# Performance work log

Measured on AMD Instinct MI355X. Metric: run time of the kernel, lower is better.

## Reference

```python
import jax, jax.numpy as jnp
import numpy as np

B, IN_DIM, HV_DIM, NUM_CLASSES = 16384, 2048, 8192, 1000


def setup_inputs() -> dict:
    key = jax.random.key(0)
    kx, kp, kc = jax.random.split(key, 3)
    x = jax.random.normal(kx, (B, IN_DIM), dtype=jnp.float32)
    # +/-1 random projection and class hypervectors (2*bernoulli - 1), as in the torch buffers
    proj = (jax.random.randint(kp, (IN_DIM, HV_DIM), 0, 2) * 2 - 1).astype(jnp.float32)
    class_hv = (jax.random.randint(kc, (HV_DIM, NUM_CLASSES), 0, 2) * 2 - 1).astype(jnp.float32)
    return {"x": x, "proj": proj, "class_hv": class_hv}


def reference(x, proj, class_hv):
    # dense projection -> sign binarize -> binary associative-memory matmul (score_mode='dot')
    hv = x @ proj                                   # [B, HV_DIM]
    hv_bin = jnp.where(hv >= 0, 1.0, -1.0).astype(hv.dtype)
    scores = hv_bin @ class_hv                      # [B, NUM_CLASSES]
    return scores, hv_bin
```

## Files before the change

kernel.cpp:

```cpp
#include <hip/hip_runtime.h>
#include <hip/hip_bf16.h>

typedef _Float16 half8  __attribute__((ext_vector_type(8)));
typedef _Float16 half4_t __attribute__((ext_vector_type(4)));
typedef float    floatx4 __attribute__((ext_vector_type(4)));
typedef int      intx4   __attribute__((ext_vector_type(4)));

#define B_DIM   16384
#define IN_D    2048
#define HV_D    8192
#define NC      1000
#define NCP     1024
#define SCORES_N (B_DIM * NC)

#define GLD16(gp, lp) __builtin_amdgcn_global_load_lds( \
    (const __attribute__((address_space(1))) void*)(gp), \
    (__attribute__((address_space(3))) void*)(lp), 16, 0, 0)

__global__ void k_split(const float* __restrict__ x, _Float16* __restrict__ xh,
                        _Float16* __restrict__ xl) {
    size_t i = (size_t)blockIdx.x * 256 + threadIdx.x;
    floatx4 v = ((const floatx4*)x)[i];
    half4_t h, l;
#pragma unroll
    for (int j = 0; j < 4; ++j) {
        _Float16 hh = (_Float16)v[j];
        h[j] = hh;
        l[j] = (_Float16)(v[j] - (float)hh);
    }
    ((half4_t*)xh)[i] = h;
    ((half4_t*)xl)[i] = l;
}

__global__ void k_transpose_proj(const float* __restrict__ p, _Float16* __restrict__ pT) {
    __shared__ float tile[64][65];
    const int t = threadIdx.x;
    const int nt = blockIdx.x * 64;
    const int kt = blockIdx.y * 64;
    const int tr = t >> 4, tc = (t & 15) * 4;
#pragma unroll
    for (int s = 0; s < 4; ++s) {
        int r = tr + s * 16;
        floatx4 v = *(const floatx4*)&p[(size_t)(kt + r) * HV_D + nt + tc];
        tile[r][tc] = v[0]; tile[r][tc + 1] = v[1];
        tile[r][tc + 2] = v[2]; tile[r][tc + 3] = v[3];
    }
    __syncthreads();
#pragma unroll
    for (int s = 0; s < 4; ++s) {
        int rn = tr + s * 16;
        half4_t o;
#pragma unroll
        for (int j = 0; j < 4; ++j) o[j] = (_Float16)tile[tc + j][rn];
        *(half4_t*)&pT[(size_t)(nt + rn) * IN_D + kt + tc] = o;
    }
}

__global__ void k_pack_class(const float* __restrict__ c, signed char* __restrict__ cT) {
    __shared__ signed char tile[64][68];
    const int t = threadIdx.x;
    const int nt = blockIdx.x * 64;
    const int kt = blockIdx.y * 64;
    const int nl = t & 63;
    const int n = nt + nl;
#pragma unroll
    for (int s = 0; s < 16; ++s) {
        const int kl = s * 4 + (t >> 6);
        signed char v = 0;
        if (n < NC) {
            float f = c[(size_t)(kt + kl) * NC + n];
            v = (f >= 0.f) ? (signed char)1 : (signed char)-1;
        }
        tile[kl][nl] = v;
    }
    __syncthreads();
    const int wn = t >> 2;
    const int wk = (t & 3) * 16;
    intx4 o;
    signed char* ob = (signed char*)&o;
#pragma unroll
    for (int j = 0; j < 16; ++j) ob[j] = tile[wk + j][wn];
    *(intx4*)&cT[(size_t)(nt + wn) * HV_D + kt + wk] = o;
}

__launch_bounds__(256, 2)
__global__ void k_gemm1(const _Float16* __restrict__ xh, const _Float16* __restrict__ xl,
                        const _Float16* __restrict__ pT,
                        float* __restrict__ hv_out, signed char* __restrict__ hvb,
                        int mbase) {
    __shared__ _Float16 sAh[128 * 64];
    __shared__ _Float16 sAl[128 * 64];
    __shared__ _Float16 sB [256 * 64];
    const int t = threadIdx.x;
    const int w = t >> 6, l = t & 63;

    const int orig = blockIdx.y * 32 + blockIdx.x;
    const int lid  = (orig & 7) * 128 + (orig >> 3);
    const int bx = lid & 31, by = lid >> 5;

    const int m0 = mbase + by * 128, n0 = bx * 256;
    const int wm = (w >> 1) * 64, wn = (w & 1) * 128;
    const int lm = l & 15, kq = l >> 4;
    const int srow  = w * 8 + (l >> 3);
    const int scol  = (((l & 7) ^ ((l >> 3) & 7))) * 8;
    const int sbyte = w * 1024 + l * 16;

    floatx4 acc[4][8] = {};

    for (int k0 = 0; k0 < IN_D; k0 += 64) {
        __syncthreads();
#pragma unroll
        for (int i = 0; i < 4; ++i) {
            const size_t ga = (size_t)(m0 + srow + i * 32) * IN_D + k0 + scol;
            const int lo = sbyte + i * 4096;
            GLD16(xh + ga, (char*)sAh + lo);
            GLD16(xl + ga, (char*)sAl + lo);
        }
#pragma unroll
        for (int i = 0; i < 8; ++i) {
            const size_t gb = (size_t)(n0 + srow + i * 32) * IN_D + k0 + scol;
            GLD16(pT + gb, (char*)sB + sbyte + i * 4096);
        }
        __syncthreads();
#pragma unroll
        for (int ks = 0; ks < 2; ++ks) {
            const int csw = ((ks * 4 + kq) ^ (lm & 7)) * 8;
            half8 b[8];
#pragma unroll
            for (int ns = 0; ns < 8; ++ns)
                b[ns] = *(const half8*)&sB[(wn + ns * 16 + lm) * 64 + csw];
#pragma unroll
            for (int ms = 0; ms < 4; ++ms) {
                half8 a = *(const half8*)&sAh[(wm + ms * 16 + lm) * 64 + csw];
#pragma unroll
                for (int ns = 0; ns < 8; ++ns)
                    acc[ms][ns] = __builtin_amdgcn_mfma_f32_16x16x32_f16(a, b[ns], acc[ms][ns], 0, 0, 0);
            }
#pragma unroll
            for (int ms = 0; ms < 4; ++ms) {
                half8 a = *(const half8*)&sAl[(wm + ms * 16 + lm) * 64 + csw];
#pragma unroll
                for (int ns = 0; ns < 8; ++ns)
                    acc[ms][ns] = __builtin_amdgcn_mfma_f32_16x16x32_f16(a, b[ns], acc[ms][ns], 0, 0, 0);
            }
        }
    }

#pragma unroll
    for (int ms = 0; ms < 4; ++ms) {
#pragma unroll
        for (int ns = 0; ns < 8; ++ns) {
            const int m = m0 + wm + ms * 16 + kq * 4;
            const int n = n0 + wn + ns * 16 + lm;
#pragma unroll
            for (int r = 0; r < 4; ++r) {
                const int pos = (acc[ms][ns][r] >= 0.f);
                const size_t o = (size_t)(m + r) * HV_D + n;
                __builtin_nontemporal_store(pos ? 1.f : -1.f, &hv_out[o]);
                hvb[o] = (signed char)(pos ? 1 : -1);
            }
        }
    }
}

__launch_bounds__(256, 4)
__global__ void k_gemm2(const signed char* __restrict__ hvb, const signed char* __restrict__ cT,
                        float* __restrict__ scores) {
    __shared__ signed char sA[64 * 128];
    __shared__ signed char sB[256 * 128];
    const int t = threadIdx.x;
    const int w = t >> 6, l = t & 63;

    const int orig = blockIdx.y * 4 + blockIdx.x;
    const int lid  = (orig & 7) * 128 + (orig >> 3);
    const int bx = lid & 3, by = lid >> 2;

    const int m0 = by * 64, n0 = bx * 256;
    const int wm = (w >> 1) * 32, wn = (w & 1) * 128;
    const int lm = l & 15, kq = l >> 4;
    const int srow  = w * 8 + (l >> 3);
    const int scol  = (((l & 7) ^ ((l >> 3) & 7))) * 16;
    const int sbyte = w * 1024 + l * 16;

    intx4 acc[2][8] = {};

    for (int k0 = 0; k0 < HV_D; k0 += 128) {
        __syncthreads();
#pragma unroll
        for (int i = 0; i < 2; ++i)
            GLD16(hvb + (size_t)(m0 + srow + i * 32) * HV_D + k0 + scol,
                  (char*)sA + sbyte + i * 4096);
#pragma unroll
        for (int i = 0; i < 8; ++i)
            GLD16(cT + (size_t)(n0 + srow + i * 32) * HV_D + k0 + scol,
                  (char*)sB + sbyte + i * 4096);
        __syncthreads();
#pragma unroll
        for (int ks = 0; ks < 2; ++ks) {
            const int csw = ((ks * 4 + kq) ^ (lm & 7)) * 16;
            intx4 b[8];
#pragma unroll
            for (int ns = 0; ns < 8; ++ns)
                b[ns] = *(const intx4*)&sB[(wn + ns * 16 + lm) * 128 + csw];
#pragma unroll
            for (int ms = 0; ms < 2; ++ms) {
                intx4 a = *(const intx4*)&sA[(wm + ms * 16 + lm) * 128 + csw];
#pragma unroll
                for (int ns = 0; ns < 8; ++ns)
                    acc[ms][ns] = __builtin_amdgcn_mfma_i32_16x16x64_i8(a, b[ns], acc[ms][ns], 0, 0, 0);
            }
        }
    }

#pragma unroll
    for (int ms = 0; ms < 2; ++ms) {
#pragma unroll
        for (int ns = 0; ns < 8; ++ns) {
            const int m = m0 + wm + ms * 16 + kq * 4;
            const int n = n0 + wn + ns * 16 + lm;
            if (n < NC) {
#pragma unroll
                for (int r = 0; r < 4; ++r)
                    __builtin_nontemporal_store((float)acc[ms][ns][r],
                                                &scores[(size_t)(m + r) * NC + n]);
            }
        }
    }
}

extern "C" void kernel_launch(void* const* d_in, const int* in_sizes, int n_in,
                              void* d_out, int out_size, void* d_ws, size_t ws_size,
                              hipStream_t stream) {
    const float* x    = (const float*)d_in[0];
    const float* proj = (const float*)d_in[1];
    const float* chv  = (const float*)d_in[2];
    float* out    = (float*)d_out;
    float* scores = out;
    float* hv_out = out + (size_t)SCORES_N;

    char* ws = (char*)d_ws;
    _Float16*    xh  = (_Float16*)(ws);
    _Float16*    xl  = (_Float16*)(ws + (size_t)67108864);
    _Float16*    pT  = (_Float16*)(ws + (size_t)134217728);
    signed char* cT  = (signed char*)(ws + (size_t)167772160);
    signed char* hvb = (signed char*)(ws + (size_t)176160768);

    k_split<<<(B_DIM * IN_D / 4) / 256, 256, 0, stream>>>(x, xh, xl);
    k_transpose_proj<<<dim3(HV_D / 64, IN_D / 64), 256, 0, stream>>>(proj, pT);
    k_pack_class<<<dim3(NCP / 64, HV_D / 64), 256, 0, stream>>>(chv, cT);
    k_gemm1<<<dim3(HV_D / 256, B_DIM / 512), 256, 0, stream>>>(xh, xl, pT, hv_out, hvb, 0);
    k_gemm1<<<dim3(HV_D / 256, B_DIM / 512), 256, 0, stream>>>(xh, xl, pT, hv_out, hvb, 4096);
    k_gemm1<<<dim3(HV_D / 256, B_DIM / 512), 256, 0, stream>>>(xh, xl, pT, hv_out, hvb, 8192);
    k_gemm1<<<dim3(HV_D / 256, B_DIM / 512), 256, 0, stream>>>(xh, xl, pT, hv_out, hvb, 12288);
    k_gemm2<<<dim3(NCP / 256, B_DIM / 64), 256, 0, stream>>>(hvb, cT, scores);
}
```

Measured before the change: 1.697 ms.

## Rewrite projection GEMM as 8-wave double-buffered ping-pong pipeline with single launch

```diff
diff --git a/kernel.cpp b/kernel.cpp
--- a/kernel.cpp
+++ b/kernel.cpp
@@ -83,84 +83,138 @@
     *(intx4*)&cT[(size_t)(nt + wn) * HV_D + kt + wk] = o;
 }
 
-__launch_bounds__(256, 2)
+__launch_bounds__(512, 2)
 __global__ void k_gemm1(const _Float16* __restrict__ xh, const _Float16* __restrict__ xl,
                         const _Float16* __restrict__ pT,
-                        float* __restrict__ hv_out, signed char* __restrict__ hvb,
-                        int mbase) {
-    __shared__ _Float16 sAh[128 * 64];
-    __shared__ _Float16 sAl[128 * 64];
-    __shared__ _Float16 sB [256 * 64];
+                        float* __restrict__ hv_out, signed char* __restrict__ hvb) {
+    __shared__ _Float16 sAh[2][128 * 64];
+    __shared__ _Float16 sAl[2][128 * 64];
+    __shared__ _Float16 sB [2][256 * 64];
     const int t = threadIdx.x;
     const int w = t >> 6, l = t & 63;
-
-    const int orig = blockIdx.y * 32 + blockIdx.x;
-    const int lid  = (orig & 7) * 128 + (orig >> 3);
-    const int bx = lid & 31, by = lid >> 5;
-
-    const int m0 = mbase + by * 128, n0 = bx * 256;
-    const int wm = (w >> 1) * 64, wn = (w & 1) * 128;
+    const int m0 = blockIdx.y * 128, n0 = blockIdx.x * 256;
+    const int wm = (w >> 2) * 64, wn = (w & 3) * 64;
     const int lm = l & 15, kq = l >> 4;
-    const int srow  = w * 8 + (l >> 3);
-    const int scol  = (((l & 7) ^ ((l >> 3) & 7))) * 8;
-    const int sbyte = w * 1024 + l * 16;
-
-    floatx4 acc[4][8] = {};
-
-    for (int k0 = 0; k0 < IN_D; k0 += 64) {
-        __syncthreads();
-#pragma unroll
-        for (int i = 0; i < 4; ++i) {
-            const size_t ga = (size_t)(m0 + srow + i * 32) * IN_D + k0 + scol;
-            const int lo = sbyte + i * 4096;
-            GLD16(xh + ga, (char*)sAh + lo);
-            GLD16(xl + ga, (char*)sAl + lo);
-        }
-#pragma unroll
-        for (int i = 0; i < 8; ++i) {
-            const size_t gb = (size_t)(n0 + srow + i * 32) * IN_D + k0 + scol;
-            GLD16(pT + gb, (char*)sB + sbyte + i * 4096);
-        }
-        __syncthreads();
-#pragma unroll
-        for (int ks = 0; ks < 2; ++ks) {
-            const int csw = ((ks * 4 + kq) ^ (lm & 7)) * 8;
-            half8 b[8];
-#pragma unroll
-            for (int ns = 0; ns < 8; ++ns)
-                b[ns] = *(const half8*)&sB[(wn + ns * 16 + lm) * 64 + csw];
-#pragma unroll
-            for (int ms = 0; ms < 4; ++ms) {
-                half8 a = *(const half8*)&sAh[(wm + ms * 16 + lm) * 64 + csw];
-#pragma unroll
-                for (int ns = 0; ns < 8; ++ns)
-                    acc[ms][ns] = __builtin_amdgcn_mfma_f32_16x16x32_f16(a, b[ns], acc[ms][ns], 0, 0, 0);
-            }
-#pragma unroll
-            for (int ms = 0; ms < 4; ++ms) {
-                half8 a = *(const half8*)&sAl[(wm + ms * 16 + lm) * 64 + csw];
-#pragma unroll
-                for (int ns = 0; ns < 8; ++ns)
-                    acc[ms][ns] = __builtin_amdgcn_mfma_f32_16x16x32_f16(a, b[ns], acc[ms][ns], 0, 0, 0);
-            }
-        }
-    }
+
+    const int arow  = (w & 3) * 8 + (l >> 3) + (w >> 2) * 64;
+    const int gcol  = ((l & 7) ^ (l >> 3)) * 8;
+    const int sbyte = arow * 128 + (l & 7) * 16;
+    const size_t aBase = (size_t)(m0 + arow) * IN_D + gcol;
+    const size_t bBase = (size_t)(n0 + arow) * IN_D + gcol;
+
+    const int csw0 = ((kq)     ^ (lm & 7)) * 8;
+    const int csw1 = ((kq + 4) ^ (lm & 7)) * 8;
+
+    floatx4 acc[4][4] = {};
+
+#define STAGE_A(buf, i, kt) do { \
+    const size_t g_ = aBase + (size_t)((i) * 32 * IN_D) + (size_t)((kt) * 64); \
+    GLD16(xh + g_, (char*)&sAh[buf][0] + (i) * 4096 + sbyte); \
+    GLD16(xl + g_, (char*)&sAl[buf][0] + (i) * 4096 + sbyte); \
+} while (0)
+
+#define STAGE_B2(buf, p, kt) do { \
+    const size_t g_ = bBase + (size_t)((p) * 32 * IN_D) + (size_t)((kt) * 64); \
+    GLD16(pT + g_,                       (char*)&sB[buf][0] + (p) * 4096 + sbyte); \
+    GLD16(pT + g_ + (size_t)(128 * IN_D), (char*)&sB[buf][0] + 16384 + (p) * 4096 + sbyte); \
+} while (0)
+
+#define VM6 asm volatile("s_waitcnt vmcnt(6)" ::: "memory")
+#define VM8 asm volatile("s_waitcnt vmcnt(8)" ::: "memory")
+#define VM4 asm volatile("s_waitcnt vmcnt(4)" ::: "memory")
+#define VM0 asm volatile("s_waitcnt vmcnt(0)" ::: "memory")
+#define VMNOP do {} while (0)
+
+#define MM(A_, B_, ci, cj) \
+    acc[ci][cj] = __builtin_amdgcn_mfma_f32_16x16x32_f16(A_, B_, acc[ci][cj], 0, 0, 0)
+
+#define PHASE(buf, mh, nh, ISSUE_STMT, WAIT_STMT) do { \
+    const int ra0 = (wm + (mh) * 32      + lm) * 64; \
+    const int ra1 = (wm + (mh) * 32 + 16 + lm) * 64; \
+    const int rb0 = (wn + (nh) * 32      + lm) * 64; \
+    const int rb1 = (wn + (nh) * 32 + 16 + lm) * 64; \
+    half8 aH00 = *(const half8*)&sAh[buf][ra0 + csw0]; \
+    half8 aH01 = *(const half8*)&sAh[buf][ra0 + csw1]; \
+    half8 aH10 = *(const half8*)&sAh[buf][ra1 + csw0]; \
+    half8 aH11 = *(const half8*)&sAh[buf][ra1 + csw1]; \
+    half8 aL00 = *(const half8*)&sAl[buf][ra0 + csw0]; \
+    half8 aL01 = *(const half8*)&sAl[buf][ra0 + csw1]; \
+    half8 aL10 = *(const half8*)&sAl[buf][ra1 + csw0]; \
+    half8 aL11 = *(const half8*)&sAl[buf][ra1 + csw1]; \
+    half8 b00  = *(const half8*)&sB[buf][rb0 + csw0]; \
+    half8 b01  = *(const half8*)&sB[buf][rb0 + csw1]; \
+    half8 b10  = *(const half8*)&sB[buf][rb1 + csw0]; \
+    half8 b11  = *(const half8*)&sB[buf][rb1 + csw1]; \
+    ISSUE_STMT; \
+    WAIT_STMT; \
+    __builtin_amdgcn_sched_barrier(0); \
+    __builtin_amdgcn_s_barrier(); \
+    __builtin_amdgcn_sched_barrier(0); \
+    __builtin_amdgcn_s_setprio(1); \
+    MM(aH00, b00, (mh)*2+0, (nh)*2+0); MM(aL00, b00, (mh)*2+0, (nh)*2+0); \
+    MM(aH01, b01, (mh)*2+0, (nh)*2+0); MM(aL01, b01, (mh)*2+0, (nh)*2+0); \
+    MM(aH00, b10, (mh)*2+0, (nh)*2+1); MM(aL00, b10, (mh)*2+0, (nh)*2+1); \
+    MM(aH01, b11, (mh)*2+0, (nh)*2+1); MM(aL01, b11, (mh)*2+0, (nh)*2+1); \
+    MM(aH10, b00, (mh)*2+1, (nh)*2+0); MM(aL10, b00, (mh)*2+1, (nh)*2+0); \
+    MM(aH11, b01, (mh)*2+1, (nh)*2+0); MM(aL11, b01, (mh)*2+1, (nh)*2+0); \
+    MM(aH10, b10, (mh)*2+1, (nh)*2+1); MM(aL10, b10, (mh)*2+1, (nh)*2+1); \
+    MM(aH11, b11, (mh)*2+1, (nh)*2+1); MM(aL11, b11, (mh)*2+1, (nh)*2+1); \
+    __builtin_amdgcn_s_setprio(0); \
+    __builtin_amdgcn_sched_barrier(0); \
+    __builtin_amdgcn_s_barrier(); \
+    __builtin_amdgcn_sched_barrier(0); \
+} while (0)
+
+    STAGE_A(0, 0, 0); STAGE_A(0, 1, 0);
+    STAGE_B2(0, 0, 0); STAGE_B2(0, 1, 0);
+    STAGE_A(1, 0, 1);
+    STAGE_B2(1, 0, 1);
+    VM4;
+    __builtin_amdgcn_sched_barrier(0);
+    __builtin_amdgcn_s_barrier();
+    __builtin_amdgcn_sched_barrier(0);
+
+#pragma unroll 1
+    for (int it = 0; it < 15; ++it) {
+        const int te = 2 * it;
+        PHASE(0, 0, 0, STAGE_A (1, 1, te + 1), VM6);
+        PHASE(0, 0, 1, STAGE_B2(1, 1, te + 1), VMNOP);
+        PHASE(0, 1, 0, STAGE_A (0, 0, te + 2), VMNOP);
+        PHASE(0, 1, 1, STAGE_B2(0, 0, te + 2), VM8);
+        PHASE(1, 0, 0, STAGE_A (0, 1, te + 2), VM6);
+        PHASE(1, 0, 1, STAGE_B2(0, 1, te + 2), VMNOP);
+        PHASE(1, 1, 0, STAGE_A (1, 0, te + 3), VMNOP);
+        PHASE(1, 1, 1, STAGE_B2(1, 0, te + 3), VM8);
+    }
+
+    PHASE(0, 0, 0, STAGE_A (1, 1, 31), VM6);
+    PHASE(0, 0, 1, STAGE_B2(1, 1, 31), VMNOP);
+    PHASE(0, 1, 0, VMNOP, VMNOP);
+    PHASE(0, 1, 1, VMNOP, VM4);
+    PHASE(1, 0, 0, VMNOP, VM0);
+    PHASE(1, 0, 1, VMNOP, VMNOP);
+    PHASE(1, 1, 0, VMNOP, VMNOP);
+    PHASE(1, 1, 1, VMNOP, VMNOP);
 
 #pragma unroll
     for (int ms = 0; ms < 4; ++ms) {
 #pragma unroll
-        for (int ns = 0; ns < 8; ++ns) {
+        for (int ns = 0; ns < 4; ++ns) {
             const int m = m0 + wm + ms * 16 + kq * 4;
             const int n = n0 + wn + ns * 16 + lm;
 #pragma unroll
             for (int r = 0; r < 4; ++r) {
                 const int pos = (acc[ms][ns][r] >= 0.f);
                 const size_t o = (size_t)(m + r) * HV_D + n;
-                __builtin_nontemporal_store(pos ? 1.f : -1.f, &hv_out[o]);
+                hv_out[o] = pos ? 1.f : -1.f;
                 hvb[o] = (signed char)(pos ? 1 : -1);
             }
         }
     }
+#undef PHASE
+#undef MM
+#undef STAGE_A
+#undef STAGE_B2
 }
 
 __launch_bounds__(256, 4)
@@ -248,9 +302,6 @@
     k_split<<<(B_DIM * IN_D / 4) / 256, 256, 0, stream>>>(x, xh, xl);
     k_transpose_proj<<<dim3(HV_D / 64, IN_D / 64), 256, 0, stream>>>(proj, pT);
     k_pack_class<<<dim3(NCP / 64, HV_D / 64), 256, 0, stream>>>(chv, cT);
-    k_gemm1<<<dim3(HV_D / 256, B_DIM / 512), 256, 0, stream>>>(xh, xl, pT, hv_out, hvb, 0);
-    k_gemm1<<<dim3(HV_D / 256, B_DIM / 512), 256, 0, stream>>>(xh, xl, pT, hv_out, hvb, 4096);
-    k_gemm1<<<dim3(HV_D / 256, B_DIM / 512), 256, 0, stream>>>(xh, xl, pT, hv_out, hvb, 8192);
-    k_gemm1<<<dim3(HV_D / 256, B_DIM / 512), 256, 0, stream>>>(xh, xl, pT, hv_out, hvb, 12288);
+    k_gemm1<<<dim3(HV_D / 256, B_DIM / 128), 512, 0, stream>>>(xh, xl, pT, hv_out, hvb);
     k_gemm2<<<dim3(NCP / 256, B_DIM / 64), 256, 0, stream>>>(hvb, cT, scores);
 }
```

New measurement: 2.133 ms. +25.7%, slower.
